# Kernel tuning notes

Measured on AMD Instinct MI355X. Metric: run time of the kernel, lower is better.

The kernel has to match this reference:

```python
import jax, jax.numpy as jnp
import numpy as np

D_MODEL = 512
NUM_HEADS = 8
D_HEAD = D_MODEL // NUM_HEADS
QMAX = 127.0  # int8 narrow-range symmetric
EPS = 1e-8


def _quant_dequant_weight(w):
    # per-output-channel symmetric int8 quant-dequant (brevitas default style)
    s = jnp.maximum(jnp.max(jnp.abs(w), axis=1, keepdims=True) / QMAX, EPS)
    return jnp.clip(jnp.round(w / s), -QMAX, QMAX) * s


def _quant_dequant_act(x):
    # per-tensor symmetric int8 quant-dequant (QuantIdentity)
    s = jnp.maximum(jnp.max(jnp.abs(x)) / QMAX, EPS)
    return jnp.clip(jnp.round(x / s), -QMAX, QMAX) * s


def _qlinear(x, w, b):
    return jnp.einsum('btd,od->bto', x, _quant_dequant_weight(w)) + b


def setup_inputs() -> dict:
    key = jax.random.key(0)
    ks = jax.random.split(key, 10)
    B, T = 2, 4096
    lim = 1.0 / np.sqrt(D_MODEL)
    mk = lambda k: jax.random.uniform(k, (D_MODEL, D_MODEL), jnp.float32, -lim, lim)
    mb = lambda k: jax.random.uniform(k, (D_MODEL,), jnp.float32, -lim, lim)
    return {
        'x': jax.random.normal(ks[0], (B, T, D_MODEL), jnp.float32),
        'mask': jax.random.randint(ks[1], (B, T), 0, 2, jnp.int32),
        'Wq': mk(ks[2]), 'bq': mb(ks[3]),
        'Wk': mk(ks[4]), 'bk': mb(ks[5]),
        'Wv': mk(ks[6]), 'bv': mb(ks[7]),
        'Wo': mk(ks[8]), 'bo': mb(ks[9]),
    }


def reference(x, mask, Wq, bq, Wk, bk, Wv, bv, Wo, bo):
    B, T, _ = x.shape
    shape = lambda t: t.reshape(B, T, NUM_HEADS, D_HEAD).transpose(0, 2, 1, 3)  # (B,H,T,dh)
    q = shape(_qlinear(x, Wq, bq))
    k = shape(_qlinear(x, Wk, bk))
    v = shape(_qlinear(x, Wv, bv))
    scores = jnp.einsum('bhtd,bhsd->bhts', q, k) / np.sqrt(D_HEAD)
    keep = (mask != 0)[:, None, None, :]  # (B,1,1,T), 0 = masked
    scores = jnp.where(keep, scores, -jnp.inf)
    attn = jax.nn.softmax(scores, axis=-1)
    ctx = jnp.einsum('bhts,bhsd->bhtd', attn, v)
    ctx = ctx.transpose(0, 2, 1, 3).reshape(B, T, D_MODEL)
    out = _qlinear(ctx, Wo, bo)
    return _quant_dequant_act(out)
```

## Files before the change

kernel.cpp:

```cpp
#include <hip/hip_runtime.h>
#include <hip/hip_bf16.h>

typedef __bf16 bf16;
typedef __bf16 bf16x8 __attribute__((ext_vector_type(8)));
typedef __bf16 bf16x4v __attribute__((ext_vector_type(4)));
typedef float f32x4 __attribute__((ext_vector_type(4)));

#define D_MODEL 512
#define T_SEQ   4096
#define NH      8
#define DH      64
#define M_ROWS  8192
#define VROW    8224
#define QK_SCALE 0.18033688011112042f

__device__ __forceinline__ void gload16(const void* g, void* l) {
  __builtin_amdgcn_global_load_lds(
      (const __attribute__((address_space(1))) unsigned int*)g,
      (__attribute__((address_space(3))) unsigned int*)l, 16, 0, 0);
}

__global__ __launch_bounds__(64) void detect_dtype(const unsigned short* __restrict__ xr,
                                                   int* __restrict__ flag)
{
  int lane = threadIdx.x;
  int cnt = 0;
  for (int i = lane; i < 4096; i += 64) {
    unsigned short u = xr[i];
    int e = (u >> 7) & 0xFF;
    bool insane = (e >= 133) || (e > 0 && e <= 96) || (e == 0 && (u & 0x7F) != 0);
    cnt += insane ? 1 : 0;
  }
#pragma unroll
  for (int off = 32; off >= 1; off >>= 1) cnt += __shfl_xor(cnt, off);
  if (lane == 0) *flag = (cnt > 400) ? 1 : 0;
}

__global__ __launch_bounds__(256) void convert_x(const void* __restrict__ xr,
                                                 const int* __restrict__ flag,
                                                 bf16* __restrict__ xb, int n)
{
  int i = (blockIdx.x * blockDim.x + threadIdx.x) * 4;
  if (i >= n) return;
  if (*flag) {
    float4 v = *(const float4*)((const float*)xr + i);
    __align__(8) bf16 o[4] = {(bf16)v.x, (bf16)v.y, (bf16)v.z, (bf16)v.w};
    *(uint2*)(xb + i) = *(uint2*)o;
  } else {
    *(uint2*)(xb + i) = *(const uint2*)((const bf16*)xr + i);
  }
}

__global__ __launch_bounds__(1024) void prep_aux(
    const void* b0, const void* b1, const void* b2, const void* b3,
    const int* __restrict__ mask,
    const int* __restrict__ flag, float* __restrict__ bf, float* __restrict__ mf)
{
  const void* ps[4] = {b0, b1, b2, b3};
  int fl = *flag;
  for (int t = threadIdx.x; t < 4 * D_MODEL; t += 1024) {
    int w = t >> 9, o = t & 511;
    bf[t] = fl ? ((const float*)ps[w])[o] : (float)((const bf16*)ps[w])[o];
  }
  for (int j = threadIdx.x; j < M_ROWS; j += 1024)
    mf[j] = mask[j] ? -16.0f : -1e30f;
}

__global__ __launch_bounds__(256) void qdq_weights(
    const void* __restrict__ Wq, const void* __restrict__ Wk,
    const void* __restrict__ Wv, const void* __restrict__ Wo,
    const int* __restrict__ flag, bf16* __restrict__ out)
{
  int wave = threadIdx.x >> 6, lane = threadIdx.x & 63;
  int gid = blockIdx.x * 4 + wave;
  int w = gid >> 9, row = gid & 511;
  const void* W = (w == 0) ? Wq : (w == 1) ? Wk : (w == 2) ? Wv : Wo;
  int fl = *flag;
  float v[8]; float amax = 0.f;
#pragma unroll
  for (int i = 0; i < 8; i++) {
    int idx = row * D_MODEL + lane + 64 * i;
    v[i] = fl ? ((const float*)W)[idx] : (float)((const bf16*)W)[idx];
    amax = fmaxf(amax, fabsf(v[i]));
  }
#pragma unroll
  for (int off = 32; off >= 1; off >>= 1) amax = fmaxf(amax, __shfl_xor(amax, off));
  float s = fmaxf(amax / 127.0f, 1e-8f);
  bf16* dst = out + (size_t)gid * D_MODEL;
#pragma unroll
  for (int i = 0; i < 8; i++) {
    float q = rintf(v[i] / s);
    q = fminf(fmaxf(q, -127.f), 127.f);
    dst[lane + 64*i] = (bf16)(q * s);
  }
}

#define LDS_STRIDE 40
__global__ __launch_bounds__(256) void gemm_qkv(
    const bf16* __restrict__ A, const bf16* __restrict__ W,
    const float* __restrict__ bias,
    bf16* __restrict__ Qh, bf16* __restrict__ Kh, bf16* __restrict__ VTP)
{
  __shared__ __align__(16) bf16 As[128 * LDS_STRIDE];
  __shared__ __align__(16) bf16 Bs[128 * LDS_STRIDE];

  const int tid = threadIdx.x;
  const int wave = tid >> 6, lane = tid & 63;
  const int lr = lane & 15, quad = lane >> 4;
  const int wm = (wave >> 1) * 64, wn = (wave & 1) * 64;
  const int m0 = blockIdx.x * 128, n0 = blockIdx.y * 128;
  const int sec = blockIdx.y >> 2;

  f32x4 acc[4][4];
#pragma unroll
  for (int i = 0; i < 4; i++)
#pragma unroll
    for (int j = 0; j < 4; j++) acc[i][j] = f32x4{0.f, 0.f, 0.f, 0.f};

  const int srow = tid >> 2;
  const int sseg = (tid & 3) * 8;

  for (int k0 = 0; k0 < D_MODEL; k0 += 32) {
#pragma unroll
    for (int i = 0; i < 2; i++) {
      int r = srow + i * 64;
      *(uint4*)&As[r * LDS_STRIDE + sseg] = *(const uint4*)(A + (size_t)(m0 + r) * D_MODEL + k0 + sseg);
      *(uint4*)&Bs[r * LDS_STRIDE + sseg] = *(const uint4*)(W + (size_t)(n0 + r) * D_MODEL + k0 + sseg);
    }
    __syncthreads();
    bf16x8 af[4], bfr[4];
#pragma unroll
    for (int mt = 0; mt < 4; mt++) af[mt]  = *(bf16x8*)&As[(wm + mt*16 + lr) * LDS_STRIDE + quad*8];
#pragma unroll
    for (int nt = 0; nt < 4; nt++) bfr[nt] = *(bf16x8*)&Bs[(wn + nt*16 + lr) * LDS_STRIDE + quad*8];
#pragma unroll
    for (int mt = 0; mt < 4; mt++)
#pragma unroll
      for (int nt = 0; nt < 4; nt++)
        acc[mt][nt] = __builtin_amdgcn_mfma_f32_16x16x32_bf16(af[mt], bfr[nt], acc[mt][nt], 0, 0, 0);
    __syncthreads();
  }

  const float scale = (sec == 0) ? QK_SCALE : 1.0f;
#pragma unroll
  for (int mt = 0; mt < 4; mt++) {
    int grow = m0 + wm + mt * 16 + quad * 4;
#pragma unroll
    for (int nt = 0; nt < 4; nt++) {
      int gcol = n0 + wn + nt * 16 + lr;
      float b = bias[gcol];
      if (sec == 2) {
        bf16x4v pk;
#pragma unroll
        for (int r = 0; r < 4; r++) pk[r] = (bf16)(acc[mt][nt][r] + b);
        *(bf16x4v*)(VTP + (size_t)(gcol - 1024) * VROW + grow) = pk;
      } else {
        bf16* dst = (sec == 0) ? Qh : Kh;
        int c = gcol & 511;
        int hh = c >> 6, c64 = c & 63;
#pragma unroll
        for (int r = 0; r < 4; r++) {
          int row = grow + r;
          int bb = row >> 12, t = row & 4095;
          dst[((size_t)(bb * NH + hh) * T_SEQ + t) * DH + c64] =
              (bf16)((acc[mt][nt][r] + b) * scale);
        }
      }
    }
  }
}

__global__ __launch_bounds__(256) void gemm_o(
    const bf16* __restrict__ A, const bf16* __restrict__ W,
    const float* __restrict__ bias,
    float* __restrict__ Cf, unsigned int* __restrict__ amaxp)
{
  __shared__ __align__(16) bf16 As[64 * LDS_STRIDE];
  __shared__ __align__(16) bf16 Bs[128 * LDS_STRIDE];
  __shared__ float wred[4];

  const int tid = threadIdx.x;
  const int wave = tid >> 6, lane = tid & 63;
  const int lr = lane & 15, quad = lane >> 4;
  const int wm = (wave >> 1) * 32, wn = (wave & 1) * 64;
  const int m0 = blockIdx.x * 64, n0 = blockIdx.y * 128;

  f32x4 acc[2][4];
#pragma unroll
  for (int i = 0; i < 2; i++)
#pragma unroll
    for (int j = 0; j < 4; j++) acc[i][j] = f32x4{0.f, 0.f, 0.f, 0.f};

  const int srow = tid >> 2;
  const int sseg = (tid & 3) * 8;

  for (int k0 = 0; k0 < D_MODEL; k0 += 32) {
    *(uint4*)&As[srow * LDS_STRIDE + sseg] = *(const uint4*)(A + (size_t)(m0 + srow) * D_MODEL + k0 + sseg);
#pragma unroll
    for (int i = 0; i < 2; i++) {
      int r = srow + i * 64;
      *(uint4*)&Bs[r * LDS_STRIDE + sseg] = *(const uint4*)(W + (size_t)(n0 + r) * D_MODEL + k0 + sseg);
    }
    __syncthreads();
    bf16x8 af[2], bfr[4];
#pragma unroll
    for (int mt = 0; mt < 2; mt++) af[mt]  = *(bf16x8*)&As[(wm + mt*16 + lr) * LDS_STRIDE + quad*8];
#pragma unroll
    for (int nt = 0; nt < 4; nt++) bfr[nt] = *(bf16x8*)&Bs[(wn + nt*16 + lr) * LDS_STRIDE + quad*8];
#pragma unroll
    for (int mt = 0; mt < 2; mt++)
#pragma unroll
      for (int nt = 0; nt < 4; nt++)
        acc[mt][nt] = __builtin_amdgcn_mfma_f32_16x16x32_bf16(af[mt], bfr[nt], acc[mt][nt], 0, 0, 0);
    __syncthreads();
  }

  float lmax = 0.f;
#pragma unroll
  for (int mt = 0; mt < 2; mt++) {
    int grow = m0 + wm + mt * 16 + quad * 4;
#pragma unroll
    for (int nt = 0; nt < 4; nt++) {
      int gcol = n0 + wn + nt * 16 + lr;
      float b = bias[gcol];
#pragma unroll
      for (int r = 0; r < 4; r++) {
        float v = acc[mt][nt][r] + b;
        Cf[(size_t)(grow + r) * D_MODEL + gcol] = v;
        lmax = fmaxf(lmax, fabsf(v));
      }
    }
  }
#pragma unroll
  for (int off = 32; off >= 1; off >>= 1) lmax = fmaxf(lmax, __shfl_xor(lmax, off));
  if (lane == 0) wred[wave] = lmax;
  __syncthreads();
  if (tid == 0) {
    float m = fmaxf(fmaxf(wred[0], wred[1]), fmaxf(wred[2], wred[3]));
    atomicMax(amaxp, __float_as_uint(m));
  }
}

#define PB_STRIDE 72
__global__ __launch_bounds__(256, 2) void attn(
    const bf16* __restrict__ Q, const bf16* __restrict__ K, const bf16* __restrict__ VT,
    const float* __restrict__ maskf, bf16* __restrict__ ctx)
{
  __shared__ __align__(16) bf16 Ks[2][64 * 64];
  __shared__ __align__(16) bf16 Vs[2][64 * 64];
  __shared__ __align__(16) float Mf[T_SEQ];
  __shared__ __align__(16) bf16 Pb[4][32 * PB_STRIDE];

  const int tid = threadIdx.x;
  const int wave = tid >> 6, lane = tid & 63;
  const int lr = lane & 15, quad = lane >> 4;
  const int i = blockIdx.x;
  const int bh = (i & 7) * 2 + ((i >> 3) & 1);
  const int qb = i >> 4;
  const int b = bh >> 3, h = bh & 7;
  const int q0 = qb * 128 + wave * 32;

  const bf16* Qb = Q + (size_t)bh * T_SEQ * DH;
  const bf16* Kb = K + (size_t)bh * T_SEQ * DH;
  const bf16* Vb = VT + (size_t)(h * DH) * VROW + (size_t)b * T_SEQ;
  const float* mb = maskf + b * T_SEQ;
  bf16* Pw = Pb[wave];

  const int phase = (qb * 2) & 63;
  int cc = phase;

#pragma unroll
  for (int ii = 0; ii < 4; ii++) {
    int g = ii * 256 + tid;
    gload16(mb + g * 4, &Mf[g * 4]);
  }
  {
    int kb = cc * 64;
#pragma unroll
    for (int ii = 0; ii < 2; ii++) {
      int s = ii * 256 + tid, row = s >> 3, sl = s & 7;
      gload16(Kb + (size_t)(kb + row) * DH + ((sl ^ (row & 7)) << 3), &Ks[0][s * 8]);
      gload16(Vb + (size_t)row * VROW + kb + ((sl ^ (row & 7)) << 3), &Vs[0][s * 8]);
    }
  }

  bf16x8 qf[2][2];
#pragma unroll
  for (int qt = 0; qt < 2; qt++) {
    const bf16* rq = Qb + (size_t)(q0 + qt * 16 + lr) * DH;
    qf[qt][0] = *(const bf16x8*)(rq + quad * 8);
    qf[qt][1] = *(const bf16x8*)(rq + 32 + quad * 8);
  }

  f32x4 O[2][4];
#pragma unroll
  for (int a = 0; a < 2; a++)
#pragma unroll
    for (int c = 0; c < 4; c++) O[a][c] = f32x4{0.f, 0.f, 0.f, 0.f};
  float lacc[2] = {0.f, 0.f};

  __syncthreads();

  int cur = 0;
  for (int j = 0; j < 64; j++) {
    const bool nxt = (j + 1) < 64;
    const int ccn = (cc + 1) & 63;

    if (nxt) {
      int kb = ccn * 64;
#pragma unroll
      for (int ii = 0; ii < 2; ii++) {
        int s = ii * 256 + tid, row = s >> 3, sl = s & 7;
        gload16(Kb + (size_t)(kb + row) * DH + ((sl ^ (row & 7)) << 3), &Ks[cur ^ 1][s * 8]);
        gload16(Vb + (size_t)row * VROW + kb + ((sl ^ (row & 7)) << 3), &Vs[cur ^ 1][s * 8]);
      }
    }

    f32x4 mk[4];
#pragma unroll
    for (int kt = 0; kt < 4; kt++)
      mk[kt] = *(const f32x4*)&Mf[cc * 64 + kt * 16 + quad * 4];

    bf16x8 kr[4][2];
#pragma unroll
    for (int kt = 0; kt < 4; kt++)
#pragma unroll
      for (int kh = 0; kh < 2; kh++)
        kr[kt][kh] = *(const bf16x8*)&Ks[cur][(kt * 16 + lr) * 64 +
                                             (((kh * 4 + quad) ^ (lr & 7)) << 3)];

#pragma unroll
    for (int qt = 0; qt < 2; qt++) {
      f32x4 z[4];
#pragma unroll
      for (int kt = 0; kt < 4; kt++) {
        f32x4 t = mk[kt];
        t = __builtin_amdgcn_mfma_f32_16x16x32_bf16(kr[kt][0], qf[qt][0], t, 0, 0, 0);
        t = __builtin_amdgcn_mfma_f32_16x16x32_bf16(kr[kt][1], qf[qt][1], t, 0, 0, 0);
        z[kt] = t;
      }
      float la = lacc[qt];
#pragma unroll
      for (int kt = 0; kt < 4; kt++) {
        bf16x4v pk;
#pragma unroll
        for (int r = 0; r < 4; r++) {
          float p = __builtin_amdgcn_exp2f(z[kt][r]);
          la += p;
          pk[r] = (bf16)p;
        }
        *(bf16x4v*)&Pw[(qt * 16 + lr) * PB_STRIDE + kt * 16 + quad * 4] = pk;
      }
      lacc[qt] = la;
    }

    bf16x8 pf[2][2];
#pragma unroll
    for (int qt = 0; qt < 2; qt++) {
      pf[qt][0] = *(bf16x8*)&Pw[(qt * 16 + lr) * PB_STRIDE + quad * 8];
      pf[qt][1] = *(bf16x8*)&Pw[(qt * 16 + lr) * PB_STRIDE + 32 + quad * 8];
    }

    bf16x8 vr[4][2];
#pragma unroll
    for (int nt = 0; nt < 4; nt++)
#pragma unroll
      for (int ks = 0; ks < 2; ks++)
        vr[nt][ks] = *(const bf16x8*)&Vs[cur][(nt * 16 + lr) * 64 +
                                             (((ks * 4 + quad) ^ (lr & 7)) << 3)];

#pragma unroll
    for (int nt = 0; nt < 4; nt++)
#pragma unroll
      for (int qt = 0; qt < 2; qt++) {
        O[qt][nt] = __builtin_amdgcn_mfma_f32_16x16x32_bf16(pf[qt][0], vr[nt][0], O[qt][nt], 0, 0, 0);
        O[qt][nt] = __builtin_amdgcn_mfma_f32_16x16x32_bf16(pf[qt][1], vr[nt][1], O[qt][nt], 0, 0, 0);
      }

    __syncthreads();
    cur ^= 1; cc = ccn;
  }

#pragma unroll
  for (int qt = 0; qt < 2; qt++) {
    float ls = lacc[qt];
    ls += __shfl_xor(ls, 16);
    ls += __shfl_xor(ls, 32);
    float linv = 1.0f / ls;
    float lO[4];
#pragma unroll
    for (int r = 0; r < 4; r++) lO[r] = __shfl(linv, quad * 4 + r);
#pragma unroll
    for (int nt = 0; nt < 4; nt++)
#pragma unroll
      for (int r = 0; r < 4; r++) {
        size_t row = (size_t)(b * T_SEQ + q0 + qt * 16 + quad * 4 + r);
        ctx[row * D_MODEL + h * DH + nt * 16 + lr] = (bf16)(O[qt][nt][r] * lO[r]);
      }
  }
}

__global__ __launch_bounds__(256) void act_qdq(
    const float* __restrict__ pre, const unsigned int* __restrict__ amaxp,
    const int* __restrict__ flag, void* __restrict__ outv, int n)
{
  int i = (blockIdx.x * blockDim.x + threadIdx.x) * 4;
  if (i >= n) return;
  float s = fmaxf(__uint_as_float(*amaxp) / 127.0f, 1e-8f);
  float4 v = *(const float4*)(pre + i);
  float o[4] = {v.x, v.y, v.z, v.w};
#pragma unroll
  for (int r = 0; r < 4; r++) {
    float q = rintf(o[r] / s);
    q = fminf(fmaxf(q, -127.f), 127.f);
    o[r] = q * s;
  }
  if (*flag) {
    *(float4*)((float*)outv + i) = make_float4(o[0], o[1], o[2], o[3]);
  } else {
    __align__(8) bf16 ob[4] = {(bf16)o[0], (bf16)o[1], (bf16)o[2], (bf16)o[3]};
    *(uint2*)((bf16*)outv + i) = *(uint2*)ob;
  }
}

extern "C" void kernel_launch(void* const* d_in, const int* in_sizes, int n_in,
                              void* d_out, int out_size, void* d_ws, size_t ws_size,
                              hipStream_t stream) {
  const void* x    = d_in[0];
  const int*  mask = (const int*)d_in[1];
  const void* Wq = d_in[2]; const void* bq = d_in[3];
  const void* Wk = d_in[4]; const void* bk = d_in[5];
  const void* Wv = d_in[6]; const void* bv = d_in[7];
  const void* Wo = d_in[8]; const void* bo = d_in[9];

  char* ws = (char*)d_ws;
  int*  flag  = (int*)(ws + 0);
  unsigned int* amax = (unsigned int*)(ws + 64);
  float* biasf = (float*)(ws + 1024);
  float* maskf = (float*)(ws + 16384);
  bf16* Wt  = (bf16*)(ws + 65536);
  bf16* xb  = (bf16*)(ws + 4194304);
  bf16* Qm  = (bf16*)(ws + 12582912);
  bf16* Km  = (bf16*)(ws + 20971520);
  bf16* VT  = (bf16*)(ws + 29360128);
  bf16* Cm  = (bf16*)(ws + 4194304);
  float* pre = (float*)(ws + 12582912);

  hipMemsetAsync(amax, 0, 4, stream);
  detect_dtype<<<1, 64, 0, stream>>>((const unsigned short*)x, flag);
  convert_x<<<4096, 256, 0, stream>>>(x, flag, xb, M_ROWS * D_MODEL);
  prep_aux<<<1, 1024, 0, stream>>>(bq, bk, bv, bo, mask, flag, biasf, maskf);
  qdq_weights<<<512, 256, 0, stream>>>(Wq, Wk, Wv, Wo, flag, Wt);
  gemm_qkv<<<dim3(64, 12), 256, 0, stream>>>(xb, Wt, biasf, Qm, Km, VT);
  attn<<<512, 256, 0, stream>>>(Qm, Km, VT, maskf, Cm);
  gemm_o<<<dim3(128, 4), 256, 0, stream>>>(Cm, Wt + 3*262144, biasf + 1536, pre, amax);
  act_qdq<<<4096, 256, 0, stream>>>(pre, amax, flag, d_out, M_ROWS * D_MODEL);
}
```

Before: 242.5 us.

## Permute K rows so softmax P stays in registers, dropping LDS round-trip

```diff
diff --git a/kernel.cpp b/kernel.cpp
--- a/kernel.cpp
+++ b/kernel.cpp
@@ -241,7 +241,6 @@
   }
 }
 
-#define PB_STRIDE 72
 __global__ __launch_bounds__(256, 2) void attn(
     const bf16* __restrict__ Q, const bf16* __restrict__ K, const bf16* __restrict__ VT,
     const float* __restrict__ maskf, bf16* __restrict__ ctx)
@@ -249,7 +248,6 @@
   __shared__ __align__(16) bf16 Ks[2][64 * 64];
   __shared__ __align__(16) bf16 Vs[2][64 * 64];
   __shared__ __align__(16) float Mf[T_SEQ];
-  __shared__ __align__(16) bf16 Pb[4][32 * PB_STRIDE];
 
   const int tid = threadIdx.x;
   const int wave = tid >> 6, lane = tid & 63;
@@ -264,10 +262,19 @@
   const bf16* Kb = K + (size_t)bh * T_SEQ * DH;
   const bf16* Vb = VT + (size_t)(h * DH) * VROW + (size_t)b * T_SEQ;
   const float* mb = maskf + b * T_SEQ;
-  bf16* Pw = Pb[wave];
 
   const int phase = (qb * 2) & 63;
   int cc = phase;
+
+  const bf16* kSrc[2]; const bf16* vSrc[2];
+#pragma unroll
+  for (int ii = 0; ii < 2; ii++) {
+    int s = ii * 256 + tid, row = s >> 3, sl = s & 7;
+    int kt = row >> 4, m = row & 15;
+    int keym = ((m >> 2) << 3) + ((kt & 1) << 2) + (m & 3) + ((kt >> 1) << 5);
+    kSrc[ii] = Kb + (size_t)keym * DH + ((sl ^ (row & 7)) << 3);
+    vSrc[ii] = Vb + (size_t)row * VROW + ((sl ^ (row & 7)) << 3);
+  }
 
 #pragma unroll
   for (int ii = 0; ii < 4; ii++) {
@@ -278,9 +285,9 @@
     int kb = cc * 64;
 #pragma unroll
     for (int ii = 0; ii < 2; ii++) {
-      int s = ii * 256 + tid, row = s >> 3, sl = s & 7;
-      gload16(Kb + (size_t)(kb + row) * DH + ((sl ^ (row & 7)) << 3), &Ks[0][s * 8]);
-      gload16(Vb + (size_t)row * VROW + kb + ((sl ^ (row & 7)) << 3), &Vs[0][s * 8]);
+      int s = ii * 256 + tid;
+      gload16(kSrc[ii] + (size_t)kb * DH, &Ks[0][s * 8]);
+      gload16(vSrc[ii] + kb, &Vs[0][s * 8]);
     }
   }
 
@@ -310,16 +317,16 @@
       int kb = ccn * 64;
 #pragma unroll
       for (int ii = 0; ii < 2; ii++) {
-        int s = ii * 256 + tid, row = s >> 3, sl = s & 7;
-        gload16(Kb + (size_t)(kb + row) * DH + ((sl ^ (row & 7)) << 3), &Ks[cur ^ 1][s * 8]);
-        gload16(Vb + (size_t)row * VROW + kb + ((sl ^ (row & 7)) << 3), &Vs[cur ^ 1][s * 8]);
+        int s = ii * 256 + tid;
+        gload16(kSrc[ii] + (size_t)kb * DH, &Ks[cur ^ 1][s * 8]);
+        gload16(vSrc[ii] + kb, &Vs[cur ^ 1][s * 8]);
       }
     }
 
     f32x4 mk[4];
 #pragma unroll
     for (int kt = 0; kt < 4; kt++)
-      mk[kt] = *(const f32x4*)&Mf[cc * 64 + kt * 16 + quad * 4];
+      mk[kt] = *(const f32x4*)&Mf[cc * 64 + ((kt >> 1) << 5) + (quad << 3) + ((kt & 1) << 2)];
 
     bf16x8 kr[4][2];
 #pragma unroll
@@ -329,6 +336,7 @@
         kr[kt][kh] = *(const bf16x8*)&Ks[cur][(kt * 16 + lr) * 64 +
                                              (((kh * 4 + quad) ^ (lr & 7)) << 3)];
 
+    bf16x8 pfa[2][2];
 #pragma unroll
     for (int qt = 0; qt < 2; qt++) {
       f32x4 z[4];
@@ -342,23 +350,14 @@
       float la = lacc[qt];
 #pragma unroll
       for (int kt = 0; kt < 4; kt++) {
-        bf16x4v pk;
 #pragma unroll
         for (int r = 0; r < 4; r++) {
           float p = __builtin_amdgcn_exp2f(z[kt][r]);
           la += p;
-          pk[r] = (bf16)p;
+          pfa[qt][kt >> 1][((kt & 1) << 2) + r] = (bf16)p;
         }
-        *(bf16x4v*)&Pw[(qt * 16 + lr) * PB_STRIDE + kt * 16 + quad * 4] = pk;
       }
       lacc[qt] = la;
-    }
-
-    bf16x8 pf[2][2];
-#pragma unroll
-    for (int qt = 0; qt < 2; qt++) {
-      pf[qt][0] = *(bf16x8*)&Pw[(qt * 16 + lr) * PB_STRIDE + quad * 8];
-      pf[qt][1] = *(bf16x8*)&Pw[(qt * 16 + lr) * PB_STRIDE + 32 + quad * 8];
     }
 
     bf16x8 vr[4][2];
@@ -373,8 +372,8 @@
     for (int nt = 0; nt < 4; nt++)
 #pragma unroll
       for (int qt = 0; qt < 2; qt++) {
-        O[qt][nt] = __builtin_amdgcn_mfma_f32_16x16x32_bf16(pf[qt][0], vr[nt][0], O[qt][nt], 0, 0, 0);
-        O[qt][nt] = __builtin_amdgcn_mfma_f32_16x16x32_bf16(pf[qt][1], vr[nt][1], O[qt][nt], 0, 0, 0);
+        O[qt][nt] = __builtin_amdgcn_mfma_f32_16x16x32_bf16(pfa[qt][0], vr[nt][0], O[qt][nt], 0, 0, 0);
+        O[qt][nt] = __builtin_amdgcn_mfma_f32_16x16x32_bf16(pfa[qt][1], vr[nt][1], O[qt][nt], 0, 0, 0);
       }
 
     __syncthreads();
```

Result: faster. 223.8 us (-7.7%).
